# Kernel optimization log

Hardware: AMD Instinct MI355X
Metric: run time of the kernel (lower is better)

## Reference

```python
import jax, jax.numpy as jnp
import numpy as np

HIDDEN = 4544
N_HEADS = 71
HEAD_DIM = 64
SEQ = 2048
ROPE_BASE = 10000.0


def _rope_cos_sin(seq_len, dim, base=ROPE_BASE):
    inv_freq = 1.0 / (base ** (jnp.arange(0, dim, 2, dtype=jnp.float32) / dim))
    t = jnp.arange(seq_len, dtype=jnp.float32)
    freqs = jnp.einsum('i,j->ij', t, inv_freq)          # [s, dim/2]
    emb = jnp.concatenate([freqs, freqs], axis=-1)      # [s, dim]
    return jnp.cos(emb), jnp.sin(emb)


def _rotate_half(x):
    x1, x2 = jnp.split(x, 2, axis=-1)
    return jnp.concatenate([-x2, x1], axis=-1)


def _apply_rope(x, cos, sin):
    # x: [..., s, d]; cos/sin: [s, d] broadcast over leading dims
    return x * cos + _rotate_half(x) * sin


def setup_inputs() -> dict:
    key = jax.random.key(0)
    k1, k2, k3 = jax.random.split(key, 3)
    hidden_states = jax.random.normal(k1, (1, 1, SEQ, HIDDEN), dtype=jnp.float32) * 0.02
    qkv_weight = jax.random.normal(k2, ((N_HEADS + 2) * HEAD_DIM, HIDDEN), dtype=jnp.float32) * 0.02
    dense_weight = jax.random.normal(k3, (HIDDEN, HIDDEN), dtype=jnp.float32) * 0.02
    # causal additive mask, same construction as the torch module (triu of -1e5)
    mask = jnp.triu(jnp.full((SEQ, SEQ), -100000.0, dtype=jnp.float32), k=1)[None, None]
    return {
        'hidden_states': hidden_states,
        'qkv_weight': qkv_weight,
        'dense_weight': dense_weight,
        'attention_mask': mask,
    }


def reference(hidden_states, qkv_weight, dense_weight, attention_mask):
    b = hidden_states.shape[0]
    s = hidden_states.shape[2]
    x = hidden_states[:, 0]                                   # [b, s, H]

    # fused QKV projection (no bias): [b, s, (nH+2)*d]
    fused = jnp.einsum('bsh,oh->bso', x, qkv_weight)

    q = fused[..., : N_HEADS * HEAD_DIM]
    q = q.reshape(b, s, N_HEADS, HEAD_DIM).transpose(0, 2, 1, 3)   # [b, nH, s, d]
    k = fused[..., N_HEADS * HEAD_DIM : (N_HEADS + 1) * HEAD_DIM]  # [b, s, d] (single KV head, MQA)
    v = fused[..., (N_HEADS + 1) * HEAD_DIM :]                     # [b, s, d]

    cos, sin = _rope_cos_sin(s, HEAD_DIM)
    q = _apply_rope(q, cos, sin)
    k = _apply_rope(k, cos, sin)

    scale = 1.0 / np.sqrt(HEAD_DIM).astype(np.float32)
    scores = jnp.einsum('bhqd,bkd->bhqk', q, k) * scale            # [b, nH, s, s]
    scores = scores + attention_mask
    attn = jax.nn.softmax(scores, axis=-1)
    out = jnp.einsum('bhqk,bkd->bhqd', attn, v)                    # [b, nH, s, d]

    out = out.transpose(0, 2, 1, 3).reshape(b, s, N_HEADS * HEAD_DIM)  # concat heads
    out = jnp.einsum('bsh,oh->bso', out, dense_weight)             # dense projection
    return out[:, None]                                            # [b, 1, s, H]
```

## Files before the change

kernel.cpp:

```cpp
#include <hip/hip_runtime.h>

#define SEQ     2048
#define HIDDEN  4544
#define NHEAD   71
#define HD      64
#define QKV_OUT 4672

typedef __bf16    bf16;
typedef _Float16  f16;
typedef __bf16    bf16x8 __attribute__((ext_vector_type(8)));
typedef __bf16    bf16x4 __attribute__((ext_vector_type(4)));
typedef _Float16  f16x4  __attribute__((ext_vector_type(4)));
typedef _Float16  f16x8  __attribute__((ext_vector_type(8)));
typedef float     f32x4  __attribute__((ext_vector_type(4)));

__device__ inline void gl2lds16(const void* g, void* ldsbase) {
  __builtin_amdgcn_global_load_lds(
      (const __attribute__((address_space(1))) unsigned int*)g,
      (__attribute__((address_space(3))) unsigned int*)ldsbase,
      16, 0, 0);
}

__global__ void cvt_f32_bf16_k(const float* __restrict__ in, bf16* __restrict__ out, int n4) {
  int i = blockIdx.x * blockDim.x + threadIdx.x;
  if (i >= n4) return;
  float4 f = ((const float4*)in)[i];
  bf16x4 o;
  o[0] = (bf16)f.x; o[1] = (bf16)f.y; o[2] = (bf16)f.z; o[3] = (bf16)f.w;
  *(bf16x4*)(out + (size_t)i * 4) = o;
}

__global__ __launch_bounds__(256) void gemm_bt_k(const bf16* __restrict__ A,
                                                 const bf16* __restrict__ B,
                                                 float* __restrict__ C,
                                                 int K, int Nmat, int ldc) {
  __shared__ bf16 lA[2][128 * 32];
  __shared__ bf16 lB[2][128 * 32];
  const int t = threadIdx.x;
  const int lane = t & 63, w = t >> 6;

  const int gx = gridDim.x;
  const int nwg = gx * gridDim.y;
  const int orig = blockIdx.y * gx + blockIdx.x;
  const int swz = (orig & 7) * (nwg >> 3) + (orig >> 3);
  const int m0 = (swz % gx) * 128;
  const int n0 = (swz / gx) * 128;

  const int wm = (w >> 1) * 64, wn = (w & 1) * 64;
  const int qi = lane & 15, grp = lane >> 4;

  const int r0 = t >> 2;
  const int c0 = (t & 3) * 8;
  const bf16* gA0 = A + (size_t)(m0 + r0) * K + c0;
  const bf16* gA1 = A + (size_t)(m0 + 64 + r0) * K + c0;
  int bR0 = n0 + r0;      if (bR0 >= Nmat) bR0 = Nmat - 1;
  int bR1 = n0 + 64 + r0; if (bR1 >= Nmat) bR1 = Nmat - 1;
  const bf16* gB0 = B + (size_t)bR0 * K + c0;
  const bf16* gB1 = B + (size_t)bR1 * K + c0;
  bf16* lA00 = &lA[0][0] + w * 512;
  bf16* lA01 = &lA[0][2048] + w * 512;
  bf16* lA10 = &lA[1][0] + w * 512;
  bf16* lA11 = &lA[1][2048] + w * 512;
  bf16* lB00 = &lB[0][0] + w * 512;
  bf16* lB01 = &lB[0][2048] + w * 512;
  bf16* lB10 = &lB[1][0] + w * 512;
  bf16* lB11 = &lB[1][2048] + w * 512;

  f32x4 acc[4][4] = {};
  for (int k0 = 0; k0 < K; k0 += 64) {
    __syncthreads();
    gl2lds16(gA0 + k0,      lA00);
    gl2lds16(gA1 + k0,      lA01);
    gl2lds16(gA0 + k0 + 32, lA10);
    gl2lds16(gA1 + k0 + 32, lA11);
    gl2lds16(gB0 + k0,      lB00);
    gl2lds16(gB1 + k0,      lB01);
    gl2lds16(gB0 + k0 + 32, lB10);
    gl2lds16(gB1 + k0 + 32, lB11);
    __syncthreads();
#pragma unroll
    for (int half = 0; half < 2; ++half) {
      bf16x8 af[4], bfv[4];
#pragma unroll
      for (int i = 0; i < 4; ++i)
        af[i] = *(const bf16x8*)&lA[half][(wm + i * 16 + qi) * 32 + grp * 8];
#pragma unroll
      for (int i = 0; i < 4; ++i)
        bfv[i] = *(const bf16x8*)&lB[half][(wn + i * 16 + qi) * 32 + grp * 8];
#pragma unroll
      for (int i = 0; i < 4; ++i)
#pragma unroll
        for (int j = 0; j < 4; ++j)
          acc[i][j] = __builtin_amdgcn_mfma_f32_16x16x32_bf16(af[i], bfv[j], acc[i][j], 0, 0, 0);
    }
  }

#pragma unroll
  for (int i = 0; i < 4; ++i) {
    const int row = m0 + wm + i * 16 + grp * 4;
#pragma unroll
    for (int j = 0; j < 4; ++j) {
      const int col = n0 + wn + j * 16 + qi;
      if (col < Nmat) {
#pragma unroll
        for (int r = 0; r < 4; ++r)
          C[(size_t)(row + r) * ldc + col] = acc[i][j][r];
      }
    }
  }
}

__global__ __launch_bounds__(256) void rope_q_k(const float* __restrict__ fused,
                                                bf16* __restrict__ Qb,
                                                float* __restrict__ cs_tab,
                                                float* __restrict__ sn_tab) {
  const int s = blockIdx.x, t = threadIdx.x;
  __shared__ float cs[64], sn[64];
  if (t < 64) {
    int i = t & 31;
    double invf = pow(10000.0, -(double)i / 32.0);
    double ang = (double)s * invf;
    float c = (float)cos(ang), n = (float)sin(ang);
    cs[t] = c; sn[t] = n;
    cs_tab[s * 64 + t] = c;
    sn_tab[s * 64 + t] = n;
  }
  __syncthreads();
  const float* row = fused + (size_t)s * QKV_OUT;
  for (int e = t; e < HIDDEN; e += 256) {
    int d = e & 63;
    float x = row[e], xp = row[e ^ 32];
    float rot = (d < 32) ? -xp : xp;
    Qb[(size_t)s * HIDDEN + e] = (bf16)((x * cs[d] + rot * sn[d]) * 0.125f);
  }
}

__global__ __launch_bounds__(64) void kvprep_k(const float* __restrict__ fused,
                                               const float* __restrict__ cs_tab,
                                               const float* __restrict__ sn_tab,
                                               bf16* __restrict__ Kf,
                                               f16* __restrict__ Vf) {
  const int t16 = blockIdx.x, lane = threadIdx.x;
  const int qi = lane & 15, grp = lane >> 4;
  const int s = t16 * 16 + qi;
  const float* krow = fused + (size_t)s * QKV_OUT + NHEAD * 64;
  const float* cs = cs_tab + s * 64;
  const float* sn = sn_tab + s * 64;
#pragma unroll
  for (int half = 0; half < 2; ++half) {
    bf16x8 o;
    const int d0 = half * 32 + grp * 8;
#pragma unroll
    for (int j = 0; j < 8; ++j) {
      int d = d0 + j;
      float x = krow[d], xp = krow[d ^ 32];
      float rot = (d < 32) ? -xp : xp;
      o[j] = (bf16)(x * cs[d] + rot * sn[d]);
    }
    *(bf16x8*)&Kf[(t16 * 2 + half) * 512 + lane * 8] = o;
  }
#pragma unroll
  for (int p = 0; p < 2; ++p) {
    f16x8 o;
#pragma unroll
    for (int h = 0; h < 2; ++h) {
      const int tt = p * 2 + h;
#pragma unroll
      for (int j = 0; j < 4; ++j)
        o[h * 4 + j] = (f16)fused[(size_t)(t16 * 16 + grp * 4 + j) * QKV_OUT + (NHEAD + 1) * 64 + tt * 16 + qi];
    }
    *(f16x8*)&Vf[t16 * 1024 + p * 512 + lane * 8] = o;
  }
}

__global__ __launch_bounds__(64) void attn_k(const bf16* __restrict__ Qb,
                                             const bf16* __restrict__ Kf,
                                             const f16*  __restrict__ Vf,
                                             bf16* __restrict__ Ao) {
  __shared__ float fl[2 * 16 * 68];
  const int h = blockIdx.y;
  const int b32 = gridDim.x - 1 - blockIdx.x;
  const int lane = threadIdx.x;
  const int qi = lane & 15, grp = lane >> 4;
  const int q0 = b32 * 32;
  const int lastT = b32 >> 1;

  bf16x8 qf[2][2];
#pragma unroll
  for (int qq = 0; qq < 2; ++qq) {
    const bf16* qb = Qb + (size_t)(q0 + qq * 16 + qi) * HIDDEN + h * 64 + grp * 8;
    qf[qq][0] = *(const bf16x8*)qb;
    qf[qq][1] = *(const bf16x8*)(qb + 32);
  }

  f32x4 o[2][4] = {};
  float l[2] = {0.f, 0.f};

  for (int kb = 0; kb <= lastT; ++kb) {
    const bf16* kfp = Kf + (size_t)kb * 4096 + lane * 8;
    bf16x8 kf[4][2];
#pragma unroll
    for (int kk = 0; kk < 4; ++kk) {
      kf[kk][0] = *(const bf16x8*)(kfp + kk * 1024);
      kf[kk][1] = *(const bf16x8*)(kfp + kk * 1024 + 512);
    }
    f32x4 s4[2][4];
#pragma unroll
    for (int qq = 0; qq < 2; ++qq)
#pragma unroll
      for (int kk = 0; kk < 4; ++kk) {
        f32x4 z = {};
        s4[qq][kk] = __builtin_amdgcn_mfma_f32_16x16x32_bf16(kf[kk][0], qf[qq][0], z, 0, 0, 0);
        s4[qq][kk] = __builtin_amdgcn_mfma_f32_16x16x32_bf16(kf[kk][1], qf[qq][1], s4[qq][kk], 0, 0, 0);
      }
    const f16* vfp = Vf + (size_t)kb * 4096 + lane * 8;
    f16x4 vf[4][4];
#pragma unroll
    for (int kk = 0; kk < 4; ++kk)
#pragma unroll
      for (int p = 0; p < 2; ++p) {
        f16x8 v8 = *(const f16x8*)(vfp + kk * 1024 + p * 512);
#pragma unroll
        for (int j = 0; j < 4; ++j) {
          vf[kk][2 * p][j]     = v8[j];
          vf[kk][2 * p + 1][j] = v8[4 + j];
        }
      }

    if (kb == lastT) {
      const int dq = q0 - kb * 64 + qi;
#pragma unroll
      for (int qq = 0; qq < 2; ++qq)
#pragma unroll
        for (int kk = 0; kk < 4; ++kk)
#pragma unroll
          for (int r = 0; r < 4; ++r)
            if (kk * 16 + grp * 4 + r > dq + qq * 16) s4[qq][kk][r] = -1e30f;
    }
    f16x4 pf[2][4];
#pragma unroll
    for (int qq = 0; qq < 2; ++qq) {
      float ls = 0.f;
#pragma unroll
      for (int kk = 0; kk < 4; ++kk) {
        float p0 = __expf(s4[qq][kk][0]), p1 = __expf(s4[qq][kk][1]);
        float p2 = __expf(s4[qq][kk][2]), p3 = __expf(s4[qq][kk][3]);
        ls += (p0 + p1) + (p2 + p3);
        pf[qq][kk][0] = (f16)p0; pf[qq][kk][1] = (f16)p1;
        pf[qq][kk][2] = (f16)p2; pf[qq][kk][3] = (f16)p3;
      }
      l[qq] += ls;
    }
#pragma unroll
    for (int qq = 0; qq < 2; ++qq)
#pragma unroll
      for (int tt = 0; tt < 4; ++tt)
#pragma unroll
        for (int kk = 0; kk < 4; ++kk)
          o[qq][tt] = __builtin_amdgcn_mfma_f32_16x16x16f16(pf[qq][kk], vf[kk][tt], o[qq][tt], 0, 0, 0);
  }

#pragma unroll
  for (int qq = 0; qq < 2; ++qq) {
    float lq = l[qq];
    lq += __shfl_xor(lq, 16);
    lq += __shfl_xor(lq, 32);
    const float inv = 1.0f / lq;
    const float i0 = __shfl(inv, grp * 4 + 0);
    const float i1 = __shfl(inv, grp * 4 + 1);
    const float i2 = __shfl(inv, grp * 4 + 2);
    const float i3 = __shfl(inv, grp * 4 + 3);
    float* flq = fl + qq * 1088;
#pragma unroll
    for (int tt = 0; tt < 4; ++tt) {
      flq[(grp * 4 + 0) * 68 + tt * 16 + qi] = o[qq][tt][0] * i0;
      flq[(grp * 4 + 1) * 68 + tt * 16 + qi] = o[qq][tt][1] * i1;
      flq[(grp * 4 + 2) * 68 + tt * 16 + qi] = o[qq][tt][2] * i2;
      flq[(grp * 4 + 3) * 68 + tt * 16 + qi] = o[qq][tt][3] * i3;
    }
  }
  __syncthreads();
  const int row = lane >> 2, c0 = (lane & 3) * 16;
#pragma unroll
  for (int qq = 0; qq < 2; ++qq) {
    const float* flq = fl + qq * 1088;
    bf16x8 w0, w1;
#pragma unroll
    for (int j = 0; j < 8; ++j) {
      w0[j] = (bf16)flq[row * 68 + c0 + j];
      w1[j] = (bf16)flq[row * 68 + c0 + 8 + j];
    }
    bf16* ob = Ao + (size_t)(q0 + qq * 16 + row) * HIDDEN + h * 64 + c0;
    *(bf16x8*)ob = w0;
    *(bf16x8*)(ob + 8) = w1;
  }
}

extern "C" void kernel_launch(void* const* d_in, const int* in_sizes, int n_in,
                              void* d_out, int out_size, void* d_ws, size_t ws_size,
                              hipStream_t stream) {
  (void)in_sizes; (void)n_in; (void)out_size; (void)ws_size;
  const float* hs   = (const float*)d_in[0];
  const float* wqkv = (const float*)d_in[1];
  const float* wd   = (const float*)d_in[2];
  float* out = (float*)d_out;

  char* ws = (char*)d_ws;
  size_t off = 0;
  auto alloc = [&](size_t b) -> char* {
    char* p = ws + off;
    off += (b + 255) & ~(size_t)255;
    return p;
  };
  bf16* Xb     = (bf16*)alloc((size_t)SEQ * HIDDEN * 2);
  bf16* Wqb    = (bf16*)alloc((size_t)QKV_OUT * HIDDEN * 2);
  bf16* Wdb    = (bf16*)alloc((size_t)HIDDEN * HIDDEN * 2);
  float* fused = (float*)alloc((size_t)SEQ * QKV_OUT * 4);
  bf16* Qb     = (bf16*)alloc((size_t)SEQ * HIDDEN * 2);
  bf16* Kf     = (bf16*)alloc((size_t)(SEQ / 16) * 1024 * 2);
  f16*  Vf     = (f16*)alloc((size_t)(SEQ / 16) * 1024 * 2);
  float* cs_tab = (float*)alloc((size_t)SEQ * 64 * 4);
  float* sn_tab = (float*)alloc((size_t)SEQ * 64 * 4);
  bf16* Ao     = (bf16*)fused;

  {
    int n4 = SEQ * HIDDEN / 4;
    cvt_f32_bf16_k<<<(n4 + 255) / 256, 256, 0, stream>>>(hs, Xb, n4);
    n4 = QKV_OUT * HIDDEN / 4;
    cvt_f32_bf16_k<<<(n4 + 255) / 256, 256, 0, stream>>>(wqkv, Wqb, n4);
    n4 = HIDDEN * HIDDEN / 4;
    cvt_f32_bf16_k<<<(n4 + 255) / 256, 256, 0, stream>>>(wd, Wdb, n4);
  }
  gemm_bt_k<<<dim3(SEQ / 128, (QKV_OUT + 127) / 128), 256, 0, stream>>>(
      Xb, Wqb, fused, HIDDEN, QKV_OUT, QKV_OUT);
  rope_q_k<<<SEQ, 256, 0, stream>>>(fused, Qb, cs_tab, sn_tab);
  kvprep_k<<<SEQ / 16, 64, 0, stream>>>(fused, cs_tab, sn_tab, Kf, Vf);
  attn_k<<<dim3(SEQ / 32, NHEAD), 64, 0, stream>>>(Qb, Kf, Vf, Ao);
  gemm_bt_k<<<dim3(SEQ / 128, (HIDDEN + 127) / 128), 256, 0, stream>>>(
      Ao, Wdb, out, HIDDEN, HIDDEN, HIDDEN);
}
```

Measured before the change: 550.0 us.

## Split-K both GEMMs into two partial buffers and fold in log2e scaling

Both GEMMs now run with a z-dimension of 2 that splits K at 2304, writing two fp32 partial outputs. The partials are summed in the rope/kvprep consumers for QKV and by a new elementwise add kernel for the dense output. The aim is more workgroups to fill the GPU, since the original grids of 16x37 and 16x36 tiles underfill the CUs. In exchange it writes and reads extra fp32 buffers and adds a kernel launch. The Q scale now includes log2(e) so softmax can use exp2f, and the Q rope loop is vectorized with float4 loads.

```diff
diff --git a/kernel.cpp b/kernel.cpp
--- a/kernel.cpp
+++ b/kernel.cpp
@@ -5,6 +5,7 @@
 #define NHEAD   71
 #define HD      64
 #define QKV_OUT 4672
+#define KSPLIT  2304
 
 typedef __bf16    bf16;
 typedef _Float16  f16;
@@ -32,12 +33,17 @@
 
 __global__ __launch_bounds__(256) void gemm_bt_k(const bf16* __restrict__ A,
                                                  const bf16* __restrict__ B,
-                                                 float* __restrict__ C,
-                                                 int K, int Nmat, int ldc) {
+                                                 float* __restrict__ C0,
+                                                 float* __restrict__ C1,
+                                                 int K, int ksplit, int Nmat, int ldc) {
   __shared__ bf16 lA[2][128 * 32];
   __shared__ bf16 lB[2][128 * 32];
   const int t = threadIdx.x;
   const int lane = t & 63, w = t >> 6;
+  const int z = blockIdx.z;
+  const int kb = z ? ksplit : 0;
+  const int ke = z ? K : ksplit;
+  float* __restrict__ C = z ? C1 : C0;
 
   const int gx = gridDim.x;
   const int nwg = gx * gridDim.y;
@@ -67,7 +73,7 @@
   bf16* lB11 = &lB[1][2048] + w * 512;
 
   f32x4 acc[4][4] = {};
-  for (int k0 = 0; k0 < K; k0 += 64) {
+  for (int k0 = kb; k0 < ke; k0 += 64) {
     __syncthreads();
     gl2lds16(gA0 + k0,      lA00);
     gl2lds16(gA1 + k0,      lA01);
@@ -110,7 +116,19 @@
   }
 }
 
-__global__ __launch_bounds__(256) void rope_q_k(const float* __restrict__ fused,
+__global__ void addf4_k(const float* __restrict__ a, const float* __restrict__ b,
+                        float* __restrict__ out, int n4) {
+  int i = blockIdx.x * blockDim.x + threadIdx.x;
+  if (i >= n4) return;
+  float4 x = ((const float4*)a)[i];
+  float4 y = ((const float4*)b)[i];
+  x.x += y.x; x.y += y.y; x.z += y.z; x.w += y.w;
+  ((float4*)out)[i] = x;
+}
+
+#define QSCALE 0.18033688f
+__global__ __launch_bounds__(256) void rope_q_k(const float* __restrict__ f0,
+                                                const float* __restrict__ f1,
                                                 bf16* __restrict__ Qb,
                                                 float* __restrict__ cs_tab,
                                                 float* __restrict__ sn_tab) {
@@ -126,16 +144,34 @@
     sn_tab[s * 64 + t] = n;
   }
   __syncthreads();
-  const float* row = fused + (size_t)s * QKV_OUT;
-  for (int e = t; e < HIDDEN; e += 256) {
-    int d = e & 63;
-    float x = row[e], xp = row[e ^ 32];
-    float rot = (d < 32) ? -xp : xp;
-    Qb[(size_t)s * HIDDEN + e] = (bf16)((x * cs[d] + rot * sn[d]) * 0.125f);
-  }
-}
-
-__global__ __launch_bounds__(64) void kvprep_k(const float* __restrict__ fused,
+  const float* r0 = f0 + (size_t)s * QKV_OUT;
+  const float* r1 = f1 + (size_t)s * QKV_OUT;
+  bf16* qrow = Qb + (size_t)s * HIDDEN;
+  for (int u = t; u < NHEAD * 8; u += 256) {
+    const int head = u >> 3, c4 = (u & 7) * 4;
+    const int e = head * 64 + c4;
+    float4 lo = *(const float4*)(r0 + e);
+    float4 lo1 = *(const float4*)(r1 + e);
+    float4 hi = *(const float4*)(r0 + e + 32);
+    float4 hi1 = *(const float4*)(r1 + e + 32);
+    lo.x += lo1.x; lo.y += lo1.y; lo.z += lo1.z; lo.w += lo1.w;
+    hi.x += hi1.x; hi.y += hi1.y; hi.z += hi1.z; hi.w += hi1.w;
+    float xl[4] = {lo.x, lo.y, lo.z, lo.w};
+    float xh[4] = {hi.x, hi.y, hi.z, hi.w};
+    bf16x4 qlo, qhi;
+#pragma unroll
+    for (int j = 0; j < 4; ++j) {
+      const float c = cs[c4 + j], n = sn[c4 + j];
+      qlo[j] = (bf16)((xl[j] * c - xh[j] * n) * QSCALE);
+      qhi[j] = (bf16)((xh[j] * c + xl[j] * n) * QSCALE);
+    }
+    *(bf16x4*)(qrow + e) = qlo;
+    *(bf16x4*)(qrow + e + 32) = qhi;
+  }
+}
+
+__global__ __launch_bounds__(64) void kvprep_k(const float* __restrict__ f0,
+                                               const float* __restrict__ f1,
                                                const float* __restrict__ cs_tab,
                                                const float* __restrict__ sn_tab,
                                                bf16* __restrict__ Kf,
@@ -143,7 +179,8 @@
   const int t16 = blockIdx.x, lane = threadIdx.x;
   const int qi = lane & 15, grp = lane >> 4;
   const int s = t16 * 16 + qi;
-  const float* krow = fused + (size_t)s * QKV_OUT + NHEAD * 64;
+  const float* krow0 = f0 + (size_t)s * QKV_OUT + NHEAD * 64;
+  const float* krow1 = f1 + (size_t)s * QKV_OUT + NHEAD * 64;
   const float* cs = cs_tab + s * 64;
   const float* sn = sn_tab + s * 64;
 #pragma unroll
@@ -153,7 +190,8 @@
 #pragma unroll
     for (int j = 0; j < 8; ++j) {
       int d = d0 + j;
-      float x = krow[d], xp = krow[d ^ 32];
+      float x = krow0[d] + krow1[d];
+      float xp = krow0[d ^ 32] + krow1[d ^ 32];
       float rot = (d < 32) ? -xp : xp;
       o[j] = (bf16)(x * cs[d] + rot * sn[d]);
     }
@@ -166,8 +204,10 @@
     for (int h = 0; h < 2; ++h) {
       const int tt = p * 2 + h;
 #pragma unroll
-      for (int j = 0; j < 4; ++j)
-        o[h * 4 + j] = (f16)fused[(size_t)(t16 * 16 + grp * 4 + j) * QKV_OUT + (NHEAD + 1) * 64 + tt * 16 + qi];
+      for (int j = 0; j < 4; ++j) {
+        const size_t idx = (size_t)(t16 * 16 + grp * 4 + j) * QKV_OUT + (NHEAD + 1) * 64 + tt * 16 + qi;
+        o[h * 4 + j] = (f16)(f0[idx] + f1[idx]);
+      }
     }
     *(f16x8*)&Vf[t16 * 1024 + p * 512 + lane * 8] = o;
   }
@@ -243,8 +283,8 @@
       float ls = 0.f;
 #pragma unroll
       for (int kk = 0; kk < 4; ++kk) {
-        float p0 = __expf(s4[qq][kk][0]), p1 = __expf(s4[qq][kk][1]);
-        float p2 = __expf(s4[qq][kk][2]), p3 = __expf(s4[qq][kk][3]);
+        float p0 = exp2f(s4[qq][kk][0]), p1 = exp2f(s4[qq][kk][1]);
+        float p2 = exp2f(s4[qq][kk][2]), p3 = exp2f(s4[qq][kk][3]);
         ls += (p0 + p1) + (p2 + p3);
         pf[qq][kk][0] = (f16)p0; pf[qq][kk][1] = (f16)p1;
         pf[qq][kk][2] = (f16)p2; pf[qq][kk][3] = (f16)p3;
@@ -315,13 +355,16 @@
   bf16* Xb     = (bf16*)alloc((size_t)SEQ * HIDDEN * 2);
   bf16* Wqb    = (bf16*)alloc((size_t)QKV_OUT * HIDDEN * 2);
   bf16* Wdb    = (bf16*)alloc((size_t)HIDDEN * HIDDEN * 2);
-  float* fused = (float*)alloc((size_t)SEQ * QKV_OUT * 4);
+  float* fused0 = (float*)alloc((size_t)SEQ * QKV_OUT * 4);
+  float* fused1 = (float*)alloc((size_t)SEQ * QKV_OUT * 4);
   bf16* Qb     = (bf16*)alloc((size_t)SEQ * HIDDEN * 2);
   bf16* Kf     = (bf16*)alloc((size_t)(SEQ / 16) * 1024 * 2);
   f16*  Vf     = (f16*)alloc((size_t)(SEQ / 16) * 1024 * 2);
   float* cs_tab = (float*)alloc((size_t)SEQ * 64 * 4);
   float* sn_tab = (float*)alloc((size_t)SEQ * 64 * 4);
-  bf16* Ao     = (bf16*)fused;
+  float* out1  = (float*)alloc((size_t)SEQ * HIDDEN * 4);
+  bf16* Ao     = (bf16*)fused0;
+  float* out0  = fused1;
 
   {
     int n4 = SEQ * HIDDEN / 4;
@@ -331,11 +374,13 @@
     n4 = HIDDEN * HIDDEN / 4;
     cvt_f32_bf16_k<<<(n4 + 255) / 256, 256, 0, stream>>>(wd, Wdb, n4);
   }
-  gemm_bt_k<<<dim3(SEQ / 128, (QKV_OUT + 127) / 128), 256, 0, stream>>>(
-      Xb, Wqb, fused, HIDDEN, QKV_OUT, QKV_OUT);
-  rope_q_k<<<SEQ, 256, 0, stream>>>(fused, Qb, cs_tab, sn_tab);
-  kvprep_k<<<SEQ / 16, 64, 0, stream>>>(fused, cs_tab, sn_tab, Kf, Vf);
+  gemm_bt_k<<<dim3(SEQ / 128, (QKV_OUT + 127) / 128, 2), 256, 0, stream>>>(
+      Xb, Wqb, fused0, fused1, HIDDEN, KSPLIT, QKV_OUT, QKV_OUT);
+  rope_q_k<<<SEQ, 256, 0, stream>>>(fused0, fused1, Qb, cs_tab, sn_tab);
+  kvprep_k<<<SEQ / 16, 64, 0, stream>>>(fused0, fused1, cs_tab, sn_tab, Kf, Vf);
   attn_k<<<dim3(SEQ / 32, NHEAD), 64, 0, stream>>>(Qb, Kf, Vf, Ao);
-  gemm_bt_k<<<dim3(SEQ / 128, (HIDDEN + 127) / 128), 256, 0, stream>>>(
-      Ao, Wdb, out, HIDDEN, HIDDEN, HIDDEN);
-}
+  gemm_bt_k<<<dim3(SEQ / 128, (HIDDEN + 127) / 128, 2), 256, 0, stream>>>(
+      Ao, Wdb, out0, out1, HIDDEN, KSPLIT, HIDDEN, HIDDEN);
+  addf4_k<<<(SEQ * HIDDEN / 4 + 255) / 256, 256, 0, stream>>>(
+      out0, out1, out, SEQ * HIDDEN / 4);
+}
```

Measured after the change: 614.8 us. 11.8% more time.

## Share K/V tiles across four waves via double-buffered LDS in attention

Applied to the files above, without the earlier changes.

The attention kernel now runs 256-thread blocks covering 128 query rows per head. Four waves share K/V tiles that are streamed into LDS with global_load_lds and double-buffered, so each tile is loaded once per block instead of once per wave and the next tile's load overlaps compute. The softmax switches to exp2 with log2(e) folded into the Q scale, the RoPE-Q kernel is vectorised with float4 loads, and the output goes straight to global memory without the LDS transpose. In exchange, waves in a block now stall at barriers, and waves with earlier causal ranges sit idle while the last wave finishes its extra tiles.

```diff
diff --git a/kernel.cpp b/kernel.cpp
--- a/kernel.cpp
+++ b/kernel.cpp
@@ -110,6 +110,7 @@
   }
 }
 
+#define QSCALE 0.18033688f
 __global__ __launch_bounds__(256) void rope_q_k(const float* __restrict__ fused,
                                                 bf16* __restrict__ Qb,
                                                 float* __restrict__ cs_tab,
@@ -126,12 +127,24 @@
     sn_tab[s * 64 + t] = n;
   }
   __syncthreads();
-  const float* row = fused + (size_t)s * QKV_OUT;
-  for (int e = t; e < HIDDEN; e += 256) {
-    int d = e & 63;
-    float x = row[e], xp = row[e ^ 32];
-    float rot = (d < 32) ? -xp : xp;
-    Qb[(size_t)s * HIDDEN + e] = (bf16)((x * cs[d] + rot * sn[d]) * 0.125f);
+  const float* r0 = fused + (size_t)s * QKV_OUT;
+  bf16* qrow = Qb + (size_t)s * HIDDEN;
+  for (int u = t; u < NHEAD * 8; u += 256) {
+    const int head = u >> 3, c4 = (u & 7) * 4;
+    const int e = head * 64 + c4;
+    float4 lo = *(const float4*)(r0 + e);
+    float4 hi = *(const float4*)(r0 + e + 32);
+    float xl[4] = {lo.x, lo.y, lo.z, lo.w};
+    float xh[4] = {hi.x, hi.y, hi.z, hi.w};
+    bf16x4 qlo, qhi;
+#pragma unroll
+    for (int j = 0; j < 4; ++j) {
+      const float c = cs[c4 + j], n = sn[c4 + j];
+      qlo[j] = (bf16)((xl[j] * c - xh[j] * n) * QSCALE);
+      qhi[j] = (bf16)((xh[j] * c + xl[j] * n) * QSCALE);
+    }
+    *(bf16x4*)(qrow + e) = qlo;
+    *(bf16x4*)(qrow + e + 32) = qhi;
   }
 }
 
@@ -173,17 +186,20 @@
   }
 }
 
-__global__ __launch_bounds__(64) void attn_k(const bf16* __restrict__ Qb,
-                                             const bf16* __restrict__ Kf,
-                                             const f16*  __restrict__ Vf,
-                                             bf16* __restrict__ Ao) {
-  __shared__ float fl[2 * 16 * 68];
+__global__ __launch_bounds__(256) void attn_k(const bf16* __restrict__ Qb,
+                                              const bf16* __restrict__ Kf,
+                                              const f16*  __restrict__ Vf,
+                                              bf16* __restrict__ Ao) {
+  __shared__ ushort kv[2][8192];
   const int h = blockIdx.y;
-  const int b32 = gridDim.x - 1 - blockIdx.x;
-  const int lane = threadIdx.x;
+  const int b128 = gridDim.x - 1 - blockIdx.x;
+  const int t = threadIdx.x;
+  const int lane = t & 63, w = t >> 6;
   const int qi = lane & 15, grp = lane >> 4;
-  const int q0 = b32 * 32;
-  const int lastT = b32 >> 1;
+  const int q0 = b128 * 128 + w * 32;
+  const int myLastT = q0 >> 6;
+  const int lastTmax = b128 * 2 + 1;
+  const size_t lo16 = (size_t)lane * 16;
 
   bf16x8 qf[2][2];
 #pragma unroll
@@ -196,68 +212,98 @@
   f32x4 o[2][4] = {};
   float l[2] = {0.f, 0.f};
 
-  for (int kb = 0; kb <= lastT; ++kb) {
-    const bf16* kfp = Kf + (size_t)kb * 4096 + lane * 8;
-    bf16x8 kf[4][2];
-#pragma unroll
-    for (int kk = 0; kk < 4; ++kk) {
-      kf[kk][0] = *(const bf16x8*)(kfp + kk * 1024);
-      kf[kk][1] = *(const bf16x8*)(kfp + kk * 1024 + 512);
-    }
-    f32x4 s4[2][4];
-#pragma unroll
-    for (int qq = 0; qq < 2; ++qq)
+  {
+    const char* kB = (const char*)Kf;
+    const char* vB = (const char*)Vf;
+    char* d = (char*)&kv[0][0];
+    gl2lds16(kB + w * 1024 + lo16,        d + w * 1024);
+    gl2lds16(kB + 4096 + w * 1024 + lo16, d + 4096 + w * 1024);
+    gl2lds16(vB + w * 1024 + lo16,        d + 8192 + w * 1024);
+    gl2lds16(vB + 4096 + w * 1024 + lo16, d + 12288 + w * 1024);
+  }
+
+  for (int kb = 0; kb <= lastTmax; ++kb) {
+    const int buf = kb & 1;
+    if (kb < lastTmax) {
+      const char* kB = (const char*)Kf + (size_t)(kb + 1) * 8192;
+      const char* vB = (const char*)Vf + (size_t)(kb + 1) * 8192;
+      char* d = (char*)&kv[buf ^ 1][0];
+      gl2lds16(kB + w * 1024 + lo16,        d + w * 1024);
+      gl2lds16(kB + 4096 + w * 1024 + lo16, d + 4096 + w * 1024);
+      gl2lds16(vB + w * 1024 + lo16,        d + 8192 + w * 1024);
+      gl2lds16(vB + 4096 + w * 1024 + lo16, d + 12288 + w * 1024);
+      asm volatile("s_waitcnt vmcnt(4)" ::: "memory");
+    } else {
+      asm volatile("s_waitcnt vmcnt(0)" ::: "memory");
+    }
+    __builtin_amdgcn_s_barrier();
+    asm volatile("" ::: "memory");
+
+    if (kb <= myLastT) {
+      const bf16* kfp = (const bf16*)&kv[buf][0] + lane * 8;
+      bf16x8 kf[4][2];
 #pragma unroll
       for (int kk = 0; kk < 4; ++kk) {
-        f32x4 z = {};
-        s4[qq][kk] = __builtin_amdgcn_mfma_f32_16x16x32_bf16(kf[kk][0], qf[qq][0], z, 0, 0, 0);
-        s4[qq][kk] = __builtin_amdgcn_mfma_f32_16x16x32_bf16(kf[kk][1], qf[qq][1], s4[qq][kk], 0, 0, 0);
+        kf[kk][0] = *(const bf16x8*)(kfp + kk * 1024);
+        kf[kk][1] = *(const bf16x8*)(kfp + kk * 1024 + 512);
       }
-    const f16* vfp = Vf + (size_t)kb * 4096 + lane * 8;
-    f16x4 vf[4][4];
-#pragma unroll
-    for (int kk = 0; kk < 4; ++kk)
-#pragma unroll
-      for (int p = 0; p < 2; ++p) {
-        f16x8 v8 = *(const f16x8*)(vfp + kk * 1024 + p * 512);
-#pragma unroll
-        for (int j = 0; j < 4; ++j) {
-          vf[kk][2 * p][j]     = v8[j];
-          vf[kk][2 * p + 1][j] = v8[4 + j];
+      f32x4 s4[2][4];
+#pragma unroll
+      for (int qq = 0; qq < 2; ++qq)
+#pragma unroll
+        for (int kk = 0; kk < 4; ++kk) {
+          f32x4 z = {};
+          s4[qq][kk] = __builtin_amdgcn_mfma_f32_16x16x32_bf16(kf[kk][0], qf[qq][0], z, 0, 0, 0);
+          s4[qq][kk] = __builtin_amdgcn_mfma_f32_16x16x32_bf16(kf[kk][1], qf[qq][1], s4[qq][kk], 0, 0, 0);
         }
+      const f16* vfp = (const f16*)((const ushort*)&kv[buf][0] + 4096) + lane * 8;
+      f16x4 vf[4][4];
+#pragma unroll
+      for (int kk = 0; kk < 4; ++kk)
+#pragma unroll
+        for (int p = 0; p < 2; ++p) {
+          f16x8 v8 = *(const f16x8*)(vfp + kk * 1024 + p * 512);
+#pragma unroll
+          for (int j = 0; j < 4; ++j) {
+            vf[kk][2 * p][j]     = v8[j];
+            vf[kk][2 * p + 1][j] = v8[4 + j];
+          }
+        }
+
+      if (kb == myLastT) {
+        const int dq = q0 - kb * 64 + qi;
+#pragma unroll
+        for (int qq = 0; qq < 2; ++qq)
+#pragma unroll
+          for (int kk = 0; kk < 4; ++kk)
+#pragma unroll
+            for (int r = 0; r < 4; ++r)
+              if (kk * 16 + grp * 4 + r > dq + qq * 16) s4[qq][kk][r] = -1e30f;
       }
-
-    if (kb == lastT) {
-      const int dq = q0 - kb * 64 + qi;
+      f16x4 pf[2][4];
+#pragma unroll
+      for (int qq = 0; qq < 2; ++qq) {
+        float ls = 0.f;
+#pragma unroll
+        for (int kk = 0; kk < 4; ++kk) {
+          float p0 = exp2f(s4[qq][kk][0]), p1 = exp2f(s4[qq][kk][1]);
+          float p2 = exp2f(s4[qq][kk][2]), p3 = exp2f(s4[qq][kk][3]);
+          ls += (p0 + p1) + (p2 + p3);
+          pf[qq][kk][0] = (f16)p0; pf[qq][kk][1] = (f16)p1;
+          pf[qq][kk][2] = (f16)p2; pf[qq][kk][3] = (f16)p3;
+        }
+        l[qq] += ls;
+      }
 #pragma unroll
       for (int qq = 0; qq < 2; ++qq)
 #pragma unroll
-        for (int kk = 0; kk < 4; ++kk)
-#pragma unroll
-          for (int r = 0; r < 4; ++r)
-            if (kk * 16 + grp * 4 + r > dq + qq * 16) s4[qq][kk][r] = -1e30f;
-    }
-    f16x4 pf[2][4];
-#pragma unroll
-    for (int qq = 0; qq < 2; ++qq) {
-      float ls = 0.f;
-#pragma unroll
-      for (int kk = 0; kk < 4; ++kk) {
-        float p0 = __expf(s4[qq][kk][0]), p1 = __expf(s4[qq][kk][1]);
-        float p2 = __expf(s4[qq][kk][2]), p3 = __expf(s4[qq][kk][3]);
-        ls += (p0 + p1) + (p2 + p3);
-        pf[qq][kk][0] = (f16)p0; pf[qq][kk][1] = (f16)p1;
-        pf[qq][kk][2] = (f16)p2; pf[qq][kk][3] = (f16)p3;
-      }
-      l[qq] += ls;
-    }
-#pragma unroll
-    for (int qq = 0; qq < 2; ++qq)
-#pragma unroll
-      for (int tt = 0; tt < 4; ++tt)
-#pragma unroll
-        for (int kk = 0; kk < 4; ++kk)
-          o[qq][tt] = __builtin_amdgcn_mfma_f32_16x16x16f16(pf[qq][kk], vf[kk][tt], o[qq][tt], 0, 0, 0);
+        for (int tt = 0; tt < 4; ++tt)
+#pragma unroll
+          for (int kk = 0; kk < 4; ++kk)
+            o[qq][tt] = __builtin_amdgcn_mfma_f32_16x16x16f16(pf[qq][kk], vf[kk][tt], o[qq][tt], 0, 0, 0);
+    }
+    asm volatile("" ::: "memory");
+    __builtin_amdgcn_s_barrier();
   }
 
 #pragma unroll
@@ -266,33 +312,17 @@
     lq += __shfl_xor(lq, 16);
     lq += __shfl_xor(lq, 32);
     const float inv = 1.0f / lq;
-    const float i0 = __shfl(inv, grp * 4 + 0);
-    const float i1 = __shfl(inv, grp * 4 + 1);
-    const float i2 = __shfl(inv, grp * 4 + 2);
-    const float i3 = __shfl(inv, grp * 4 + 3);
-    float* flq = fl + qq * 1088;
-#pragma unroll
-    for (int tt = 0; tt < 4; ++tt) {
-      flq[(grp * 4 + 0) * 68 + tt * 16 + qi] = o[qq][tt][0] * i0;
-      flq[(grp * 4 + 1) * 68 + tt * 16 + qi] = o[qq][tt][1] * i1;
-      flq[(grp * 4 + 2) * 68 + tt * 16 + qi] = o[qq][tt][2] * i2;
-      flq[(grp * 4 + 3) * 68 + tt * 16 + qi] = o[qq][tt][3] * i3;
-    }
-  }
-  __syncthreads();
-  const int row = lane >> 2, c0 = (lane & 3) * 16;
-#pragma unroll
-  for (int qq = 0; qq < 2; ++qq) {
-    const float* flq = fl + qq * 1088;
-    bf16x8 w0, w1;
-#pragma unroll
-    for (int j = 0; j < 8; ++j) {
-      w0[j] = (bf16)flq[row * 68 + c0 + j];
-      w1[j] = (bf16)flq[row * 68 + c0 + 8 + j];
-    }
-    bf16* ob = Ao + (size_t)(q0 + qq * 16 + row) * HIDDEN + h * 64 + c0;
-    *(bf16x8*)ob = w0;
-    *(bf16x8*)(ob + 8) = w1;
+    float ir[4];
+#pragma unroll
+    for (int r = 0; r < 4; ++r) ir[r] = __shfl(inv, grp * 4 + r);
+#pragma unroll
+    for (int r = 0; r < 4; ++r) {
+      const int row = q0 + qq * 16 + grp * 4 + r;
+      bf16* ob = Ao + (size_t)row * HIDDEN + h * 64 + qi;
+#pragma unroll
+      for (int tt = 0; tt < 4; ++tt)
+        ob[tt * 16] = (bf16)(o[qq][tt][r] * ir[r]);
+    }
   }
 }
 
@@ -335,7 +365,7 @@
       Xb, Wqb, fused, HIDDEN, QKV_OUT, QKV_OUT);
   rope_q_k<<<SEQ, 256, 0, stream>>>(fused, Qb, cs_tab, sn_tab);
   kvprep_k<<<SEQ / 16, 64, 0, stream>>>(fused, cs_tab, sn_tab, Kf, Vf);
-  attn_k<<<dim3(SEQ / 32, NHEAD), 64, 0, stream>>>(Qb, Kf, Vf, Ao);
+  attn_k<<<dim3(SEQ / 128, NHEAD), 256, 0, stream>>>(Qb, Kf, Vf, Ao);
   gemm_bt_k<<<dim3(SEQ / 128, (HIDDEN + 127) / 128), 256, 0, stream>>>(
       Ao, Wdb, out, HIDDEN, HIDDEN, HIDDEN);
 }
```

Result: slower. 610.1 us (+10.9%).

## Double-buffer K loads in attention loop, vectorize RoPE, use exp2 softmax

Applied to the files above, without the earlier changes.

The attention kernel now prefetches the next K tile into a second register buffer while the current tile is computed, so global load latency overlaps with the MFMA work. The RoPE kernel processes four elements per thread with float4 loads and bf16x4 stores, pairing each low half with its high half directly. The Q scale now folds in log2(e) so the softmax can use exp2f instead of __expf. The extra K register buffer raises register pressure and may lower occupancy.

```diff
diff --git a/kernel.cpp b/kernel.cpp
--- a/kernel.cpp
+++ b/kernel.cpp
@@ -110,6 +110,7 @@
   }
 }
 
+#define QSCALE 0.18033688f
 __global__ __launch_bounds__(256) void rope_q_k(const float* __restrict__ fused,
                                                 bf16* __restrict__ Qb,
                                                 float* __restrict__ cs_tab,
@@ -126,12 +127,24 @@
     sn_tab[s * 64 + t] = n;
   }
   __syncthreads();
-  const float* row = fused + (size_t)s * QKV_OUT;
-  for (int e = t; e < HIDDEN; e += 256) {
-    int d = e & 63;
-    float x = row[e], xp = row[e ^ 32];
-    float rot = (d < 32) ? -xp : xp;
-    Qb[(size_t)s * HIDDEN + e] = (bf16)((x * cs[d] + rot * sn[d]) * 0.125f);
+  const float* r0 = fused + (size_t)s * QKV_OUT;
+  bf16* qrow = Qb + (size_t)s * HIDDEN;
+  for (int u = t; u < NHEAD * 8; u += 256) {
+    const int head = u >> 3, c4 = (u & 7) * 4;
+    const int e = head * 64 + c4;
+    float4 lo = *(const float4*)(r0 + e);
+    float4 hi = *(const float4*)(r0 + e + 32);
+    float xl[4] = {lo.x, lo.y, lo.z, lo.w};
+    float xh[4] = {hi.x, hi.y, hi.z, hi.w};
+    bf16x4 qlo, qhi;
+#pragma unroll
+    for (int j = 0; j < 4; ++j) {
+      const float c = cs[c4 + j], n = sn[c4 + j];
+      qlo[j] = (bf16)((xl[j] * c - xh[j] * n) * QSCALE);
+      qhi[j] = (bf16)((xh[j] * c + xl[j] * n) * QSCALE);
+    }
+    *(bf16x4*)(qrow + e) = qlo;
+    *(bf16x4*)(qrow + e + 32) = qhi;
   }
 }
 
@@ -196,14 +209,16 @@
   f32x4 o[2][4] = {};
   float l[2] = {0.f, 0.f};
 
-  for (int kb = 0; kb <= lastT; ++kb) {
-    const bf16* kfp = Kf + (size_t)kb * 4096 + lane * 8;
-    bf16x8 kf[4][2];
+  auto loadK = [&](bf16x8 (&dst)[4][2], int T) {
+    const bf16* p = Kf + (size_t)T * 4096 + lane * 8;
 #pragma unroll
     for (int kk = 0; kk < 4; ++kk) {
-      kf[kk][0] = *(const bf16x8*)(kfp + kk * 1024);
-      kf[kk][1] = *(const bf16x8*)(kfp + kk * 1024 + 512);
-    }
+      dst[kk][0] = *(const bf16x8*)(p + kk * 1024);
+      dst[kk][1] = *(const bf16x8*)(p + kk * 1024 + 512);
+    }
+  };
+
+  auto compute = [&](bf16x8 (&kf)[4][2], int kb) {
     f32x4 s4[2][4];
 #pragma unroll
     for (int qq = 0; qq < 2; ++qq)
@@ -243,8 +258,8 @@
       float ls = 0.f;
 #pragma unroll
       for (int kk = 0; kk < 4; ++kk) {
-        float p0 = __expf(s4[qq][kk][0]), p1 = __expf(s4[qq][kk][1]);
-        float p2 = __expf(s4[qq][kk][2]), p3 = __expf(s4[qq][kk][3]);
+        float p0 = exp2f(s4[qq][kk][0]), p1 = exp2f(s4[qq][kk][1]);
+        float p2 = exp2f(s4[qq][kk][2]), p3 = exp2f(s4[qq][kk][3]);
         ls += (p0 + p1) + (p2 + p3);
         pf[qq][kk][0] = (f16)p0; pf[qq][kk][1] = (f16)p1;
         pf[qq][kk][2] = (f16)p2; pf[qq][kk][3] = (f16)p3;
@@ -258,6 +273,18 @@
 #pragma unroll
         for (int kk = 0; kk < 4; ++kk)
           o[qq][tt] = __builtin_amdgcn_mfma_f32_16x16x16f16(pf[qq][kk], vf[kk][tt], o[qq][tt], 0, 0, 0);
+  };
+
+  bf16x8 kA[4][2], kB[4][2];
+  loadK(kA, 0);
+  int kb = 0;
+  for (;;) {
+    if (kb < lastT) loadK(kB, kb + 1);
+    compute(kA, kb);
+    if (++kb > lastT) break;
+    if (kb < lastT) loadK(kA, kb + 1);
+    compute(kB, kb);
+    if (++kb > lastT) break;
   }
 
 #pragma unroll
```

Result: slower. 593.6 us (+7.9%).
